# Kernel optimization log

Measured on AMD Instinct MI355X. Metric: run time of the kernel, lower is better.

## Reference

```python
import jax, jax.numpy as jnp
import numpy as np

B, M, HID, NH = 2, 2048, 1024, 16
D = HID // NH  # 64


def setup_inputs() -> dict:
    key = jax.random.key(0)
    ks = jax.random.split(key, 6)
    s = 0.02  # weight init scale
    return {
        "h": jax.random.normal(ks[0], (B, M, HID), dtype=jnp.float32),
        "key_pe": jax.random.normal(ks[1], (1, D, M), dtype=jnp.float32) * s,
        "Wq": jax.random.normal(ks[2], (HID, HID), dtype=jnp.float32) * s,
        "Wk": jax.random.normal(ks[3], (HID, HID), dtype=jnp.float32) * s,
        "Wv": jax.random.normal(ks[4], (HID, HID), dtype=jnp.float32) * s,
        "Wo": jax.random.normal(ks[5], (HID, HID), dtype=jnp.float32) * s,
    }


def reference(h, key_pe, Wq, Wk, Wv, Wo):
    # Faithful to the source: in SelfAttention.forward the gathered-span scores
    # are overwritten by dense Q K^T, and the softmaxed `attn` is discarded;
    # the returned value is (Q K^T) V (no scaling, no softmax). key_pe only
    # feeds the dead softmax branch, so it does not affect the output.
    b, m, hd = h.shape
    nh, d = NH, hd // NH

    def heads(x):  # (B, M, HID) -> (B, NH, M, D)
        return x.reshape(b, m, nh, d).transpose(0, 2, 1, 3)

    q = heads(h @ Wq.T)
    k = heads(h @ Wk.T)
    v = heads(h @ Wv.T)

    attn_cont = jnp.einsum("bhqd,bhkd->bhqk", q, k)  # (B, NH, M, M)
    out = jnp.einsum("bhqk,bhkd->bhqd", attn_cont, v)  # (B, NH, M, D)
    out = out.transpose(0, 2, 1, 3).reshape(b, m, hd)  # (B, M, HID)
    return out @ Wo.T
```

## Files before the change

kernel.cpp:

```cpp
#include <hip/hip_runtime.h>
#include <hip/hip_bf16.h>


typedef unsigned short u16;
typedef unsigned int u32;
typedef __attribute__((ext_vector_type(8))) short bf16x8;
typedef __attribute__((ext_vector_type(4))) float f32x4;

__device__ __forceinline__ void async_copy16(void* lds, const void* g) {
  __builtin_amdgcn_global_load_lds((const __attribute__((address_space(1))) void*)g,
                                   (__attribute__((address_space(3))) void*)lds,
                                   16, 0, 0);
}

__device__ __forceinline__ u16 f2bf(float f) {
  union { __hip_bfloat16 h; u16 u; } c;
  c.h = __float2bfloat16(f);
  return c.u;
}
__device__ __forceinline__ float bflo(u32 w) {
  union { u32 u; float f; } c; c.u = w << 16; return c.f;
}
__device__ __forceinline__ float bfhi(u32 w) {
  union { u32 u; float f; } c; c.u = w & 0xFFFF0000u; return c.f;
}
__device__ __forceinline__ ushort4 cvt4(float4 v) {
  ushort4 o; o.x = f2bf(v.x); o.y = f2bf(v.y); o.z = f2bf(v.z); o.w = f2bf(v.w);
  return o;
}

__global__ __launch_bounds__(256) void prep(const float4* __restrict__ h,
                                            const float4* __restrict__ wq,
                                            const float4* __restrict__ wk,
                                            const float4* __restrict__ wv,
                                            ushort4* __restrict__ hb,
                                            ushort4* __restrict__ wcat) {
  int i = blockIdx.x * 256 + threadIdx.x;
  if (i < 1048576) { hb[i] = cvt4(h[i]); return; }
  i -= 1048576;
  if (i < 262144) { wcat[i] = cvt4(wq[i]); return; }
  i -= 262144;
  if (i < 262144) { wcat[262144 + i] = cvt4(wk[i]); return; }
  i -= 262144;
  wcat[524288 + i] = cvt4(wv[i]);
}

template <bool BF16_OUT, int BM, int BN>
__global__ __launch_bounds__(256) void gemm_bt(const u16* __restrict__ A, int lda,
                                               const u16* __restrict__ B0,
                                               const u16* __restrict__ B1,
                                               void* __restrict__ Cv,
                                               int N, int K) {
  constexpr int WR = BM / 64;
  constexpr int WC = 4 / WR;
  constexpr int NI = BN / WC / 16;
  __shared__ u16 Als[BM * 64];
  __shared__ u16 Bls[BN * 64];
  const int t = threadIdx.x;
  const int lane = t & 63;
  const int wave = t >> 6;
  const int wm = (wave / WC) * 64;
  const int wn = (wave % WC) * (BN / WC);
  const int lrow = lane & 15;
  const int quad = lane >> 4;
  const int m0 = blockIdx.y * BM;
  const int n0 = blockIdx.x * BN;
  const u16* B = (B1 != nullptr && m0 >= 2048) ? B1 : B0;

  const int srow = t >> 3;
  const int scol = (((t & 7) ^ (srow & 7)) * 8);
  const u16* Ag0 = A + (size_t)(m0 + srow) * lda + scol;
  const u16* Bg0 = B + (size_t)(n0 + srow) * K + scol;
  u16* Al0 = Als + t * 8;
  u16* Bl0 = Bls + t * 8;

  f32x4 acc[4][NI];
#pragma unroll
  for (int i = 0; i < 4; ++i)
#pragma unroll
    for (int j = 0; j < NI; ++j) acc[i][j] = {0.f, 0.f, 0.f, 0.f};

  for (int k0 = 0; k0 < K; k0 += 64) {
#pragma unroll
    for (int c = 0; c < BM / 32; ++c)
      async_copy16(Al0 + c * 2048, Ag0 + (size_t)(c * 32) * lda + k0);
#pragma unroll
    for (int c = 0; c < BN / 32; ++c)
      async_copy16(Bl0 + c * 2048, Bg0 + (size_t)(c * 32) * K + k0);
    __syncthreads();

#pragma unroll
    for (int half = 0; half < 2; ++half) {
      const int gg = quad + half * 4;
      bf16x8 af[4], bfv[NI];
#pragma unroll
      for (int i = 0; i < 4; ++i) {
        const int ra = wm + i * 16 + lrow;
        af[i] = *(const bf16x8*)(Als + ra * 64 + ((gg ^ (ra & 7)) << 3));
      }
#pragma unroll
      for (int i = 0; i < NI; ++i) {
        const int rb = wn + i * 16 + lrow;
        bfv[i] = *(const bf16x8*)(Bls + rb * 64 + ((gg ^ (rb & 7)) << 3));
      }
#pragma unroll
      for (int mi = 0; mi < 4; ++mi)
#pragma unroll
        for (int ni = 0; ni < NI; ++ni)
          acc[mi][ni] = __builtin_amdgcn_mfma_f32_16x16x32_bf16(
              af[mi], bfv[ni], acc[mi][ni], 0, 0, 0);
    }
    __syncthreads();
  }

  const int crow0 = m0 + wm + (lane >> 4) * 4;
  const int ccol0 = n0 + wn + (lane & 15);
#pragma unroll
  for (int mi = 0; mi < 4; ++mi)
#pragma unroll
    for (int ni = 0; ni < NI; ++ni) {
      const int col = ccol0 + ni * 16;
#pragma unroll
      for (int r = 0; r < 4; ++r) {
        const size_t idx = (size_t)(crow0 + mi * 16 + r) * N + col;
        if (BF16_OUT) ((u16*)Cv)[idx]   = f2bf(acc[mi][ni][r]);
        else          ((float*)Cv)[idx] = acc[mi][ni][r];
      }
    }
}

__global__ __launch_bounds__(256) void s_kernel(const u16* __restrict__ QKV,
                                                float* __restrict__ Spart) {
  const int bh = blockIdx.x;
  const int b = bh >> 4, hh = bh & 15;
  const int row0 = b * 2048 + blockIdx.y * 128;
  const u16* Kg = QKV + (size_t)row0 * 3072 + 1024 + hh * 64;

  __shared__ float Ks[64][64];
  __shared__ float Vs[64][64];
  const int t = threadIdx.x;
  const int lr = t >> 2;
  const int lc = (t & 3) * 16;
  const int d1 = (t >> 4) * 4;
  const int d2 = (t & 15) * 4;

  float acc[4][4] = {};

  for (int r0 = 0; r0 < 128; r0 += 64) {
    const u16* kp = Kg + (size_t)(r0 + lr) * 3072 + lc;
    const uint4 kw0 = *(const uint4*)kp;
    const uint4 kw1 = *(const uint4*)(kp + 8);
    const uint4 vw0 = *(const uint4*)(kp + 1024);
    const uint4 vw1 = *(const uint4*)(kp + 1032);
    __syncthreads();
    float* kd = &Ks[lr][lc];
    *(float4*)(kd)      = float4{bflo(kw0.x), bfhi(kw0.x), bflo(kw0.y), bfhi(kw0.y)};
    *(float4*)(kd + 4)  = float4{bflo(kw0.z), bfhi(kw0.z), bflo(kw0.w), bfhi(kw0.w)};
    *(float4*)(kd + 8)  = float4{bflo(kw1.x), bfhi(kw1.x), bflo(kw1.y), bfhi(kw1.y)};
    *(float4*)(kd + 12) = float4{bflo(kw1.z), bfhi(kw1.z), bflo(kw1.w), bfhi(kw1.w)};
    float* vd = &Vs[lr][lc];
    *(float4*)(vd)      = float4{bflo(vw0.x), bfhi(vw0.x), bflo(vw0.y), bfhi(vw0.y)};
    *(float4*)(vd + 4)  = float4{bflo(vw0.z), bfhi(vw0.z), bflo(vw0.w), bfhi(vw0.w)};
    *(float4*)(vd + 8)  = float4{bflo(vw1.x), bfhi(vw1.x), bflo(vw1.y), bfhi(vw1.y)};
    *(float4*)(vd + 12) = float4{bflo(vw1.z), bfhi(vw1.z), bflo(vw1.w), bfhi(vw1.w)};
    __syncthreads();
#pragma unroll
    for (int r = 0; r < 64; ++r) {
      float kv[4], vv[4];
      *(float4*)kv = *(const float4*)&Ks[r][d1];
      *(float4*)vv = *(const float4*)&Vs[r][d2];
#pragma unroll
      for (int i = 0; i < 4; ++i)
#pragma unroll
        for (int j = 0; j < 4; ++j) acc[i][j] += kv[i] * vv[j];
    }
  }
  float* Sp = Spart + ((size_t)bh * 16 + blockIdx.y) * 4096;
#pragma unroll
  for (int i = 0; i < 4; ++i)
    *(float4*)&Sp[(d1 + i) * 64 + d2] =
        float4{acc[i][0], acc[i][1], acc[i][2], acc[i][3]};
}

__global__ __launch_bounds__(256) void reduce_s(const float4* __restrict__ Spart,
                                                float4* __restrict__ S) {
  const int g = blockIdx.x * 256 + threadIdx.x;
  const int bh = g >> 10, j = g & 1023;
  const float4* p = Spart + (size_t)bh * 16384 + j;
  float4 a = {0.f, 0.f, 0.f, 0.f};
#pragma unroll
  for (int c = 0; c < 16; ++c) {
    const float4 v = p[(size_t)c * 1024];
    a.x += v.x; a.y += v.y; a.z += v.z; a.w += v.w;
  }
  S[g] = a;
}

__global__ __launch_bounds__(256) void t_kernel(const float* __restrict__ S,
                                                const float* __restrict__ Wo,
                                                u16* __restrict__ Tt) {
  const int n0 = blockIdx.x * 128;
  const int hh = blockIdx.y;
  const int b  = blockIdx.z;
  __shared__ float Ss[64][68];
  __shared__ float Ws[128][68];
  const int t = threadIdx.x;
  {
    const float* sg = S + (size_t)(b * 16 + hh) * 4096 + (t >> 2) * 64 + (t & 3) * 16;
    float* sd = &Ss[t >> 2][(t & 3) * 16];
#pragma unroll
    for (int i = 0; i < 4; ++i) *(float4*)(sd + 4 * i) = *(const float4*)(sg + 4 * i);
    const float* wg = Wo + (size_t)(n0 + (t >> 1)) * 1024 + hh * 64 + (t & 1) * 32;
    float* wd = &Ws[t >> 1][(t & 1) * 32];
#pragma unroll
    for (int i = 0; i < 8; ++i) *(float4*)(wd + 4 * i) = *(const float4*)(wg + 4 * i);
  }
  __syncthreads();

  const int td = (t >> 4) * 4;
  const int tn = t & 15;
  float acc[4][8] = {};
  for (int jj = 0; jj < 64; jj += 4) {
    float4 sv[4], wv[8];
#pragma unroll
    for (int i = 0; i < 4; ++i) sv[i] = *(const float4*)&Ss[td + i][jj];
#pragma unroll
    for (int k = 0; k < 8; ++k) wv[k] = *(const float4*)&Ws[tn + 16 * k][jj];
#pragma unroll
    for (int i = 0; i < 4; ++i)
#pragma unroll
      for (int k = 0; k < 8; ++k)
        acc[i][k] += sv[i].x * wv[k].x + sv[i].y * wv[k].y +
                     sv[i].z * wv[k].z + sv[i].w * wv[k].w;
  }

  u16* tp = Tt + (size_t)b * 1048576;
#pragma unroll
  for (int k = 0; k < 8; ++k) {
    const int n = n0 + tn + 16 * k;
    ushort4 o;
    o.x = f2bf(acc[0][k]); o.y = f2bf(acc[1][k]);
    o.z = f2bf(acc[2][k]); o.w = f2bf(acc[3][k]);
    *(ushort4*)&tp[(size_t)n * 1024 + hh * 64 + td] = o;
  }
}

extern "C" void kernel_launch(void* const* d_in, const int* in_sizes, int n_in,
                              void* d_out, int out_size, void* d_ws, size_t ws_size,
                              hipStream_t stream) {
  const float* h  = (const float*)d_in[0];
  const float* Wq = (const float*)d_in[2];
  const float* Wk = (const float*)d_in[3];
  const float* Wv = (const float*)d_in[4];
  const float* Wo = (const float*)d_in[5];

  char* ws = (char*)d_ws;
  u16*   hb    = (u16*)(ws);
  u16*   wcat  = (u16*)(ws + (8ull  << 20));
  u16*   QKVb  = (u16*)(ws + (16ull << 20));
  float* S     = (float*)(ws + (40ull << 20));
  u16*   Tt    = (u16*)(ws + (41ull << 20));
  float* Spart = (float*)(ws + (48ull << 20));

  prep<<<7168, 256, 0, stream>>>((const float4*)h, (const float4*)Wq,
                                 (const float4*)Wk, (const float4*)Wv,
                                 (ushort4*)hb, (ushort4*)wcat);
  gemm_bt<true, 128, 128><<<dim3(24, 32), 256, 0, stream>>>(
      hb, 1024, wcat, nullptr, QKVb, 3072, 1024);
  s_kernel<<<dim3(32, 16), 256, 0, stream>>>(QKVb, Spart);
  reduce_s<<<128, 256, 0, stream>>>((const float4*)Spart, (float4*)S);
  t_kernel<<<dim3(8, 16, 2), 256, 0, stream>>>(S, Wo, Tt);
  gemm_bt<false, 64, 128><<<dim3(8, 64), 256, 0, stream>>>(
      QKVb, 3072, Tt, Tt + 1048576, d_out, 1024, 1024);
}
```

Before: 159.9 us.

## Replace QKV projection GEMM with 256x256-tile, 8-wave pipelined kernel

Adds a dedicated gemm256 kernel for the QKV projection (4096x3072x1024). It uses 256x256 block tiles, 512 threads, double-buffered LDS loaded through async global_load_lds, and XCD-aware block mapping. Each k-step is split into four phases that interleave the next tile's loads with MFMA work, using explicit vmcnt waits, barriers and setprio. The aim is more data reuse per block and better overlap of loads with compute. In exchange the code is hardcoded to these shapes and launches only 192 blocks, which may leave some CUs idle.

```diff
diff --git a/kernel.cpp b/kernel.cpp
--- a/kernel.cpp
+++ b/kernel.cpp
@@ -43,6 +43,134 @@
   if (i < 262144) { wcat[262144 + i] = cvt4(wk[i]); return; }
   i -= 262144;
   wcat[524288 + i] = cvt4(wv[i]);
+}
+
+
+#define VW(N) asm volatile("s_waitcnt vmcnt(" #N ")" ::: "memory")
+#define NOPW ((void)0)
+
+#define GPHASE(MH, NH, STAGE, VWAIT)                                         \
+  do {                                                                       \
+    bf16x8 af[4][2], bv[2][2];                                               \
+    const u16* Ab = &Als[cur][(wm + (MH) * 64) * 64];                        \
+    const u16* Bb = &Bls[cur][(wn + (NH) * 32) * 64];                        \
+    _Pragma("unroll") for (int i = 0; i < 4; ++i) {                          \
+      af[i][0] = *(const bf16x8*)(Ab + i * 1024 + aoff0);                    \
+      af[i][1] = *(const bf16x8*)(Ab + i * 1024 + aoff1);                    \
+    }                                                                        \
+    _Pragma("unroll") for (int j = 0; j < 2; ++j) {                          \
+      bv[j][0] = *(const bf16x8*)(Bb + j * 1024 + aoff0);                    \
+      bv[j][1] = *(const bf16x8*)(Bb + j * 1024 + aoff1);                    \
+    }                                                                        \
+    STAGE;                                                                   \
+    __builtin_amdgcn_s_barrier();                                            \
+    asm volatile("s_waitcnt lgkmcnt(0)" ::: "memory");                       \
+    __builtin_amdgcn_sched_barrier(0);                                       \
+    __builtin_amdgcn_s_setprio(1);                                           \
+    _Pragma("unroll") for (int i = 0; i < 4; ++i)                            \
+        _Pragma("unroll") for (int j = 0; j < 2; ++j)                        \
+            acc[(MH) * 4 + i][(NH) * 2 + j] =                                \
+                __builtin_amdgcn_mfma_f32_16x16x32_bf16(                     \
+                    af[i][0], bv[j][0], acc[(MH) * 4 + i][(NH) * 2 + j],     \
+                    0, 0, 0);                                                \
+    _Pragma("unroll") for (int i = 0; i < 4; ++i)                            \
+        _Pragma("unroll") for (int j = 0; j < 2; ++j)                        \
+            acc[(MH) * 4 + i][(NH) * 2 + j] =                                \
+                __builtin_amdgcn_mfma_f32_16x16x32_bf16(                     \
+                    af[i][1], bv[j][1], acc[(MH) * 4 + i][(NH) * 2 + j],     \
+                    0, 0, 0);                                                \
+    __builtin_amdgcn_s_setprio(0);                                           \
+    VWAIT;                                                                   \
+    __builtin_amdgcn_s_barrier();                                            \
+  } while (0)
+
+__global__ __launch_bounds__(512, 2) void gemm256(const u16* __restrict__ A,
+                                                  const u16* __restrict__ B,
+                                                  u16* __restrict__ C) {
+  __shared__ u16 Als[2][16384];
+  __shared__ u16 Bls[2][16384];
+  const int t = threadIdx.x;
+  const int lane = t & 63;
+  const int wave = t >> 6;
+  const int wm = (wave >> 2) * 128;
+  const int wn = (wave & 3) * 64;
+  const int lrow = lane & 15;
+  const int quad = lane >> 4;
+
+  const int bid = blockIdx.x;
+  const int xcd = bid & 7;
+  const int c8 = bid >> 3;
+  const int m0 = (xcd * 2 + (c8 >= 12 ? 1 : 0)) * 256;
+  const int n0 = (c8 >= 12 ? c8 - 12 : c8) * 256;
+
+  const int lro = lane >> 3;
+  const int lgrp = (lane & 7) ^ lro;
+  const u16* Ag = A + (size_t)(m0 + lro) * 1024 + lgrp * 8;
+  const u16* Bg = B + (size_t)(n0 + lro) * 1024 + lgrp * 8;
+  const int lds_t = lane * 8;
+
+  const int sw = lrow & 7;
+  const int aoff0 = lrow * 64 + ((quad + 0) ^ sw) * 8;
+  const int aoff1 = lrow * 64 + ((quad + 4) ^ sw) * 8;
+
+  f32x4 acc[8][4];
+#pragma unroll
+  for (int i = 0; i < 8; ++i)
+#pragma unroll
+    for (int j = 0; j < 4; ++j) acc[i][j] = {0.f, 0.f, 0.f, 0.f};
+
+  auto stA = [&](int buf, int h, int kt) {
+#pragma unroll
+    for (int j = 0; j < 2; ++j) {
+      const int cx = wave * 2 + j;
+      const int rowb = h * 64 + (cx & 7) * 8 + (cx >> 3) * 128;
+      async_copy16(&Als[buf][rowb * 64 + lds_t], Ag + (size_t)rowb * 1024 + kt * 64);
+    }
+  };
+  auto stB = [&](int buf, int h, int kt) {
+#pragma unroll
+    for (int j = 0; j < 2; ++j) {
+      const int cx = wave * 2 + j;
+      const int rowb = h * 32 + (cx >> 2) * 64 + (cx & 3) * 8;
+      async_copy16(&Bls[buf][rowb * 64 + lds_t], Bg + (size_t)rowb * 1024 + kt * 64);
+    }
+  };
+
+  stA(0, 0, 0); stB(0, 0, 0); stA(0, 1, 0); stB(0, 1, 0);
+  stA(1, 0, 1); stB(1, 0, 1);
+  VW(8);
+  __builtin_amdgcn_s_barrier();
+
+  int cur = 0;
+#pragma unroll 1
+  for (int kt = 0; kt < 14; ++kt) {
+    const int nxt = cur ^ 1;
+    GPHASE(0, 0, stA(nxt, 1, kt + 1), VW(6));
+    GPHASE(0, 1, stB(nxt, 1, kt + 1), NOPW);
+    GPHASE(1, 0, stA(cur, 0, kt + 2), NOPW);
+    GPHASE(1, 1, stB(cur, 0, kt + 2), VW(8));
+    cur = nxt;
+  }
+  GPHASE(0, 0, stA(1, 1, 15), VW(6));
+  GPHASE(0, 1, stB(1, 1, 15), NOPW);
+  GPHASE(1, 0, NOPW,          NOPW);
+  GPHASE(1, 1, NOPW,          VW(4));
+  cur = 1;
+  GPHASE(0, 0, NOPW, VW(0));
+  GPHASE(0, 1, NOPW, NOPW);
+  GPHASE(1, 0, NOPW, NOPW);
+  GPHASE(1, 1, NOPW, NOPW);
+
+  const int crow0 = m0 + wm + quad * 4;
+  const int ccol0 = n0 + wn + lrow;
+#pragma unroll
+  for (int mf = 0; mf < 8; ++mf)
+#pragma unroll
+    for (int nf = 0; nf < 4; ++nf)
+#pragma unroll
+      for (int r = 0; r < 4; ++r)
+        C[(size_t)(crow0 + mf * 16 + r) * 3072 + ccol0 + nf * 16] =
+            f2bf(acc[mf][nf][r]);
 }
 
 template <bool BF16_OUT, int BM, int BN>
@@ -265,8 +393,7 @@
   prep<<<7168, 256, 0, stream>>>((const float4*)h, (const float4*)Wq,
                                  (const float4*)Wk, (const float4*)Wv,
                                  (ushort4*)hb, (ushort4*)wcat);
-  gemm_bt<true, 128, 128><<<dim3(24, 32), 256, 0, stream>>>(
-      hb, 1024, wcat, nullptr, QKVb, 3072, 1024);
+  gemm256<<<192, 512, 0, stream>>>(hb, wcat, QKVb);
   s_kernel<<<dim3(32, 16), 256, 0, stream>>>(QKVb, Spart);
   reduce_s<<<128, 256, 0, stream>>>((const float4*)Spart, (float4*)S);
   t_kernel<<<dim3(8, 16, 2), 256, 0, stream>>>(S, Wo, Tt);
```

New measurement: 171.5 us. 1.07x slower.

## Replace QKV projection GEMM with 256x256-tile, 4-stage async pipelined kernel

Applied to the files above, without the earlier changes.

Adds a dedicated gemm256 kernel for the 4096x3072x1024 QKV projection. It uses 512-thread blocks with 256x256 output tiles, a 4-deep LDS ring filled by async global-to-LDS copies, swizzled LDS layout, raised wave priority during MFMA bursts, and an XCD-aware block-to-tile mapping. The aim is higher MFMA utilization and data reuse than the generic 128x128 gemm_bt. In exchange it uses 64KB of LDS per block and a large accumulator register set, which limits occupancy. It also launches only 192 blocks, which may leave some CUs idle.

```diff
diff --git a/kernel.cpp b/kernel.cpp
--- a/kernel.cpp
+++ b/kernel.cpp
@@ -43,6 +43,101 @@
   if (i < 262144) { wcat[262144 + i] = cvt4(wk[i]); return; }
   i -= 262144;
   wcat[524288 + i] = cvt4(wv[i]);
+}
+
+
+#define VW(N) asm volatile("s_waitcnt vmcnt(" #N ")" ::: "memory")
+#define NOPW ((void)0)
+
+#define PHASE(KT, DO_STAGE, VWAIT)                                           \
+  do {                                                                       \
+    const u16* Ab = &Als[(KT) & 3][wm * 32 + aoff];                          \
+    const u16* Bb = &Bls[(KT) & 3][wn * 32 + aoff];                          \
+    bf16x8 af[8], bv[4];                                                     \
+    _Pragma("unroll") for (int i = 0; i < 8; ++i)                            \
+        af[i] = *(const bf16x8*)(Ab + i * 512);                              \
+    _Pragma("unroll") for (int j = 0; j < 4; ++j)                            \
+        bv[j] = *(const bf16x8*)(Bb + j * 512);                              \
+    DO_STAGE;                                                                \
+    asm volatile("s_waitcnt lgkmcnt(0)" ::: "memory");                       \
+    __builtin_amdgcn_sched_barrier(0);                                       \
+    __builtin_amdgcn_s_setprio(1);                                           \
+    _Pragma("unroll") for (int i = 0; i < 8; ++i)                            \
+        _Pragma("unroll") for (int j = 0; j < 4; ++j)                        \
+            acc[i][j] = __builtin_amdgcn_mfma_f32_16x16x32_bf16(             \
+                af[i], bv[j], acc[i][j], 0, 0, 0);                           \
+    __builtin_amdgcn_s_setprio(0);                                           \
+    VWAIT;                                                                   \
+    __builtin_amdgcn_s_barrier();                                            \
+  } while (0)
+
+__global__ __launch_bounds__(512, 2) void gemm256(const u16* __restrict__ A,
+                                                  const u16* __restrict__ B,
+                                                  u16* __restrict__ C) {
+  __shared__ u16 Als[4][8192];
+  __shared__ u16 Bls[4][8192];
+  const int t = threadIdx.x;
+  const int lane = t & 63;
+  const int wave = t >> 6;
+  const int wm = (wave >> 2) * 128;
+  const int wn = (wave & 3) * 64;
+  const int lrow = lane & 15;
+  const int quad = lane >> 4;
+
+  const int bid = blockIdx.x;
+  const int xcd = bid & 7;
+  const int c8 = bid >> 3;
+  const int m0 = (xcd * 2 + (c8 >= 12 ? 1 : 0)) * 256;
+  const int n0 = (c8 >= 12 ? c8 - 12 : c8) * 256;
+
+  const int srow = lane >> 2;
+  const int sgk  = (lane & 3) ^ ((lane >> 3) & 3);
+  const u16* Ag = A + (size_t)(m0 + 32 * wave + srow) * 1024 + sgk * 8;
+  const u16* Bg = B + (size_t)(n0 + 32 * wave + srow) * 1024 + sgk * 8;
+
+  const int swz = (lrow >> 1) & 3;
+  const int aoff = lrow * 32 + ((quad ^ swz) << 3);
+
+  f32x4 acc[8][4];
+#pragma unroll
+  for (int i = 0; i < 8; ++i)
+#pragma unroll
+    for (int j = 0; j < 4; ++j) acc[i][j] = {0.f, 0.f, 0.f, 0.f};
+
+  auto stage = [&](int kt) {
+    const int buf = kt & 3;
+#pragma unroll
+    for (int j = 0; j < 2; ++j) {
+      const int rb = (32 * wave + 16 * j) * 32;
+      async_copy16(&Als[buf][rb + lane * 8],
+                   Ag + (size_t)(16 * j) * 1024 + kt * 32);
+      async_copy16(&Bls[buf][rb + lane * 8],
+                   Bg + (size_t)(16 * j) * 1024 + kt * 32);
+    }
+  };
+
+  stage(0); stage(1); stage(2);
+  VW(8);
+  __builtin_amdgcn_s_barrier();
+
+#pragma unroll 1
+  for (int kt = 0; kt < 29; ++kt) {
+    PHASE(kt, stage(kt + 3), VW(8));
+  }
+  PHASE(29, NOPW, VW(4));
+  PHASE(30, NOPW, VW(0));
+  PHASE(31, NOPW, NOPW);
+
+  const int crow0 = m0 + wm + quad * 4;
+  const int ccol0 = n0 + wn + lrow;
+#pragma unroll
+  for (int mf = 0; mf < 8; ++mf)
+#pragma unroll
+    for (int nf = 0; nf < 4; ++nf)
+#pragma unroll
+      for (int r = 0; r < 4; ++r)
+        C[(size_t)(crow0 + mf * 16 + r) * 3072 + ccol0 + nf * 16] =
+            f2bf(acc[mf][nf][r]);
 }
 
 template <bool BF16_OUT, int BM, int BN>
@@ -265,8 +360,7 @@
   prep<<<7168, 256, 0, stream>>>((const float4*)h, (const float4*)Wq,
                                  (const float4*)Wk, (const float4*)Wv,
                                  (ushort4*)hb, (ushort4*)wcat);
-  gemm_bt<true, 128, 128><<<dim3(24, 32), 256, 0, stream>>>(
-      hb, 1024, wcat, nullptr, QKVb, 3072, 1024);
+  gemm256<<<192, 512, 0, stream>>>(hb, wcat, QKVb);
   s_kernel<<<dim3(32, 16), 256, 0, stream>>>(QKVb, Spart);
   reduce_s<<<128, 256, 0, stream>>>((const float4*)Spart, (float4*)S);
   t_kernel<<<dim3(8, 16, 2), 256, 0, stream>>>(S, Wo, Tt);
```

Measured after the change: 157.1 us. About the same (-1.8%).

## Replace GEMM with 4-stage async-pipelined 512-thread kernel and XCD-aware tile mapping

Applied to the files above, without the earlier changes.

Both GEMMs move from a single-buffered 64-deep K loop, which syncs twice per tile, to a new kernel. It uses a 4-buffer LDS ring with 32-deep K tiles, prefetches three stages ahead, and waits on explicit vmcnt counts and s_barrier instead of __syncthreads. The kernel runs 512 threads with larger N tiles (384 for the QKV projection) and raises wave priority around the MFMA block. Block IDs are remapped so each XCD handles a contiguous group of row tiles, for better L2 locality. The new code hardcodes K=1024 and the grid shape, which adds complexity and makes the kernel specific to these dimensions.

```diff
diff --git a/kernel.cpp b/kernel.cpp
--- a/kernel.cpp
+++ b/kernel.cpp
@@ -27,6 +27,13 @@
 __device__ __forceinline__ ushort4 cvt4(float4 v) {
   ushort4 o; o.x = f2bf(v.x); o.y = f2bf(v.y); o.z = f2bf(v.z); o.w = f2bf(v.w);
   return o;
+}
+
+template <int N> __device__ __forceinline__ void vw() {
+  if constexpr (N == 8)      asm volatile("s_waitcnt vmcnt(8)" ::: "memory");
+  else if constexpr (N == 4) asm volatile("s_waitcnt vmcnt(4)" ::: "memory");
+  else if constexpr (N == 2) asm volatile("s_waitcnt vmcnt(2)" ::: "memory");
+  else if constexpr (N == 0) asm volatile("s_waitcnt vmcnt(0)" ::: "memory");
 }
 
 __global__ __launch_bounds__(256) void prep(const float4* __restrict__ h,
@@ -45,88 +52,115 @@
   wcat[524288 + i] = cvt4(wv[i]);
 }
 
-template <bool BF16_OUT, int BM, int BN>
-__global__ __launch_bounds__(256) void gemm_bt(const u16* __restrict__ A, int lda,
-                                               const u16* __restrict__ B0,
-                                               const u16* __restrict__ B1,
-                                               void* __restrict__ Cv,
-                                               int N, int K) {
-  constexpr int WR = BM / 64;
-  constexpr int WC = 4 / WR;
-  constexpr int NI = BN / WC / 16;
-  __shared__ u16 Als[BM * 64];
-  __shared__ u16 Bls[BN * 64];
+
+#define NOPW ((void)0)
+
+#define PHASE(KT, DO_STAGE, VWAIT)                                           \
+  do {                                                                       \
+    const u16* Ab = &Als[(KT) & 3][wm * 32 + aoff];                          \
+    const u16* Bb = &Bls[(KT) & 3][wn * 32 + aoff];                          \
+    bf16x8 af[MI], bv[NI];                                                   \
+    _Pragma("unroll") for (int i = 0; i < MI; ++i)                           \
+        af[i] = *(const bf16x8*)(Ab + i * 512);                              \
+    _Pragma("unroll") for (int j = 0; j < NI; ++j)                           \
+        bv[j] = *(const bf16x8*)(Bb + j * 512);                              \
+    DO_STAGE;                                                                \
+    asm volatile("s_waitcnt lgkmcnt(0)" ::: "memory");                       \
+    __builtin_amdgcn_sched_barrier(0);                                       \
+    __builtin_amdgcn_s_setprio(1);                                           \
+    _Pragma("unroll") for (int i = 0; i < MI; ++i)                           \
+        _Pragma("unroll") for (int j = 0; j < NI; ++j)                       \
+            acc[i][j] = __builtin_amdgcn_mfma_f32_16x16x32_bf16(             \
+                af[i], bv[j], acc[i][j], 0, 0, 0);                           \
+    __builtin_amdgcn_s_setprio(0);                                           \
+    VWAIT;                                                                   \
+    __builtin_amdgcn_s_barrier();                                            \
+  } while (0)
+
+template <bool BF16_OUT, int BN>
+__global__ __launch_bounds__(512, 2) void gemm32(const u16* __restrict__ A,
+                                                 int lda,
+                                                 const u16* __restrict__ B0,
+                                                 const u16* __restrict__ B1,
+                                                 void* __restrict__ Cv,
+                                                 int N) {
+  constexpr int SA = 1;
+  constexpr int SB = BN / 128;
+  constexpr int V  = SA + SB;
+  constexpr int MI = 4;
+  constexpr int NI = BN / 4 / 16;
+
+  __shared__ u16 Als[4][128 * 32];
+  __shared__ u16 Bls[4][BN * 32];
   const int t = threadIdx.x;
   const int lane = t & 63;
   const int wave = t >> 6;
-  const int wm = (wave / WC) * 64;
-  const int wn = (wave % WC) * (BN / WC);
+  const int wm = (wave >> 2) * 64;
+  const int wn = (wave & 3) * (BN / 4);
   const int lrow = lane & 15;
   const int quad = lane >> 4;
-  const int m0 = blockIdx.y * BM;
-  const int n0 = blockIdx.x * BN;
+
+  const int bid = blockIdx.x;
+  const int xcd = bid & 7;
+  const int c = bid >> 3;
+  const int m0 = (xcd * 4 + (c >> 3)) * 128;
+  const int n0 = (c & 7) * BN;
   const u16* B = (B1 != nullptr && m0 >= 2048) ? B1 : B0;
 
-  const int srow = t >> 3;
-  const int scol = (((t & 7) ^ (srow & 7)) * 8);
-  const u16* Ag0 = A + (size_t)(m0 + srow) * lda + scol;
-  const u16* Bg0 = B + (size_t)(n0 + srow) * K + scol;
-  u16* Al0 = Als + t * 8;
-  u16* Bl0 = Bls + t * 8;
-
-  f32x4 acc[4][NI];
-#pragma unroll
-  for (int i = 0; i < 4; ++i)
+  const int srow = lane >> 2;
+  const int sgk  = (lane & 3) ^ ((lane >> 3) & 3);
+  const u16* Ag = A + (size_t)(m0 + wave * (SA * 16) + srow) * lda + sgk * 8;
+  const u16* Bg = B + (size_t)(n0 + wave * (SB * 16) + srow) * 1024 + sgk * 8;
+
+  const int swz = (lrow >> 1) & 3;
+  const int aoff = lrow * 32 + ((quad ^ swz) << 3);
+
+  f32x4 acc[MI][NI];
+#pragma unroll
+  for (int i = 0; i < MI; ++i)
 #pragma unroll
     for (int j = 0; j < NI; ++j) acc[i][j] = {0.f, 0.f, 0.f, 0.f};
 
-  for (int k0 = 0; k0 < K; k0 += 64) {
-#pragma unroll
-    for (int c = 0; c < BM / 32; ++c)
-      async_copy16(Al0 + c * 2048, Ag0 + (size_t)(c * 32) * lda + k0);
-#pragma unroll
-    for (int c = 0; c < BN / 32; ++c)
-      async_copy16(Bl0 + c * 2048, Bg0 + (size_t)(c * 32) * K + k0);
-    __syncthreads();
-
-#pragma unroll
-    for (int half = 0; half < 2; ++half) {
-      const int gg = quad + half * 4;
-      bf16x8 af[4], bfv[NI];
-#pragma unroll
-      for (int i = 0; i < 4; ++i) {
-        const int ra = wm + i * 16 + lrow;
-        af[i] = *(const bf16x8*)(Als + ra * 64 + ((gg ^ (ra & 7)) << 3));
+  auto stage = [&](int kt) {
+    const int buf = kt & 3;
+#pragma unroll
+    for (int j = 0; j < SA; ++j) {
+      const int ch = wave * SA + j;
+      async_copy16(&Als[buf][ch * 512 + lane * 8],
+                   Ag + (size_t)(j * 16) * lda + kt * 32);
+    }
+#pragma unroll
+    for (int j = 0; j < SB; ++j) {
+      const int ch = wave * SB + j;
+      async_copy16(&Bls[buf][ch * 512 + lane * 8],
+                   Bg + (size_t)(j * 16) * 1024 + kt * 32);
+    }
+  };
+
+  stage(0); stage(1); stage(2);
+  vw<2 * V>();
+  __builtin_amdgcn_s_barrier();
+
+#pragma unroll 1
+  for (int kt = 0; kt < 29; ++kt) {
+    PHASE(kt, stage(kt + 3), vw<2 * V>());
+  }
+  PHASE(29, NOPW, vw<V>());
+  PHASE(30, NOPW, vw<0>());
+  PHASE(31, NOPW, NOPW);
+
+  const int crow0 = m0 + wm + quad * 4;
+  const int ccol0 = n0 + wn + lrow;
+#pragma unroll
+  for (int mf = 0; mf < MI; ++mf)
+#pragma unroll
+    for (int nf = 0; nf < NI; ++nf)
+#pragma unroll
+      for (int r = 0; r < 4; ++r) {
+        const size_t idx = (size_t)(crow0 + mf * 16 + r) * N + ccol0 + nf * 16;
+        if (BF16_OUT) ((u16*)Cv)[idx]   = f2bf(acc[mf][nf][r]);
+        else          ((float*)Cv)[idx] = acc[mf][nf][r];
       }
-#pragma unroll
-      for (int i = 0; i < NI; ++i) {
-        const int rb = wn + i * 16 + lrow;
-        bfv[i] = *(const bf16x8*)(Bls + rb * 64 + ((gg ^ (rb & 7)) << 3));
-      }
-#pragma unroll
-      for (int mi = 0; mi < 4; ++mi)
-#pragma unroll
-        for (int ni = 0; ni < NI; ++ni)
-          acc[mi][ni] = __builtin_amdgcn_mfma_f32_16x16x32_bf16(
-              af[mi], bfv[ni], acc[mi][ni], 0, 0, 0);
-    }
-    __syncthreads();
-  }
-
-  const int crow0 = m0 + wm + (lane >> 4) * 4;
-  const int ccol0 = n0 + wn + (lane & 15);
-#pragma unroll
-  for (int mi = 0; mi < 4; ++mi)
-#pragma unroll
-    for (int ni = 0; ni < NI; ++ni) {
-      const int col = ccol0 + ni * 16;
-#pragma unroll
-      for (int r = 0; r < 4; ++r) {
-        const size_t idx = (size_t)(crow0 + mi * 16 + r) * N + col;
-        if (BF16_OUT) ((u16*)Cv)[idx]   = f2bf(acc[mi][ni][r]);
-        else          ((float*)Cv)[idx] = acc[mi][ni][r];
-      }
-    }
 }
 
 __global__ __launch_bounds__(256) void s_kernel(const u16* __restrict__ QKV,
@@ -265,11 +299,11 @@
   prep<<<7168, 256, 0, stream>>>((const float4*)h, (const float4*)Wq,
                                  (const float4*)Wk, (const float4*)Wv,
                                  (ushort4*)hb, (ushort4*)wcat);
-  gemm_bt<true, 128, 128><<<dim3(24, 32), 256, 0, stream>>>(
-      hb, 1024, wcat, nullptr, QKVb, 3072, 1024);
+  gemm32<true, 384><<<256, 512, 0, stream>>>(hb, 1024, wcat, nullptr,
+                                             QKVb, 3072);
   s_kernel<<<dim3(32, 16), 256, 0, stream>>>(QKVb, Spart);
   reduce_s<<<128, 256, 0, stream>>>((const float4*)Spart, (float4*)S);
   t_kernel<<<dim3(8, 16, 2), 256, 0, stream>>>(S, Wo, Tt);
-  gemm_bt<false, 64, 128><<<dim3(8, 64), 256, 0, stream>>>(
-      QKVb, 3072, Tt, Tt + 1048576, d_out, 1024, 1024);
-}
+  gemm32<false, 128><<<256, 512, 0, stream>>>(QKVb, 3072, Tt, Tt + 1048576,
+                                              d_out, 1024);
+}
```

Measured after the change: 151.5 us. 1.06x faster.
